# Performance work log

Hardware: AMD Instinct MI355X
Metric: run time of the kernel (lower is better)

Reference implementation:

```python
import jax, jax.numpy as jnp
import numpy as np

NUM_HEADS = 8
FREQ_RATIO = 0.5

def setup_inputs() -> dict:
    key = jax.random.key(0)
    ks = jax.random.split(key, 4)
    B, T, J, C = 16, 256, 17, 512
    x = jax.random.normal(ks[0], (B, T, J, C), jnp.float32)
    w_qkv = jax.random.normal(ks[1], (3 * C, C), jnp.float32) * 0.02
    w_proj = jax.random.normal(ks[2], (C, C), jnp.float32) * 0.02
    b_proj = jnp.zeros((C,), jnp.float32)
    freq_gate = jnp.ones((1,), jnp.float32)
    return {"x": x, "w_qkv": w_qkv, "w_proj": w_proj, "b_proj": b_proj, "freq_gate": freq_gate}

def reference(x, w_qkv, w_proj, b_proj, freq_gate):
    B, T, J, C = x.shape
    H = NUM_HEADS
    hd = C // H
    scale = hd ** (-0.5)
    # qkv projection (no bias): [B,T,J,3,H,hd] -> [3,B,H,T,J,hd]
    qkv = (x @ w_qkv.T).reshape(B, T, J, 3, H, hd)
    qkv = jnp.transpose(qkv, (3, 0, 4, 1, 2, 5))
    q, k, v = qkv[0], qkv[1], qkv[2]
    # temporal layout: [B,H,J,T,hd]
    qt = jnp.swapaxes(q, 2, 3)
    kt = jnp.swapaxes(k, 2, 3)
    vt = jnp.swapaxes(v, 2, 3)
    # ---- time-domain temporal attention ----
    attn = jax.nn.softmax(jnp.einsum('bhjtd,bhjsd->bhjts', qt, kt) * scale, axis=-1)
    x_time = jnp.einsum('bhjts,bhjsd->bhjtd', attn, vt)
    x_time = jnp.transpose(x_time, (0, 3, 2, 1, 4)).reshape(B, T, J, C)
    # ---- frequency-domain temporal attention ----
    qf = jnp.fft.rfft(qt, axis=3)
    kf = jnp.fft.rfft(kt, axis=3)
    vf = jnp.fft.rfft(vt, axis=3)
    f_full = T // 2 + 1
    keep = max(1, int(f_full * FREQ_RATIO))  # low-frequency crop
    qf, kf, vf = qf[:, :, :, :keep], kf[:, :, :, :keep], vf[:, :, :, :keep]
    af = jnp.einsum('bhjfd,bhjgd->bhjfg', qf, jnp.conj(kf)) * scale  # complex [B,H,J,keep,keep]
    af = jax.nn.softmax(af.real, axis=-1) + 1j * jax.nn.softmax(af.imag, axis=-1)
    xf = jnp.einsum('bhjfg,bhjgd->bhjfd', af, vf)
    xf = jnp.pad(xf, ((0, 0), (0, 0), (0, 0), (0, f_full - keep), (0, 0)))  # zero-pad high freqs
    x_freq = jnp.fft.irfft(xf, n=T, axis=3)
    x_freq = jnp.transpose(x_freq, (0, 3, 2, 1, 4)).reshape(B, T, J, C)
    # ---- gated combine + output projection ----
    gate = jax.nn.sigmoid(freq_gate)[0]
    out = gate * x_freq + (1.0 - gate) * x_time
    return out @ w_proj.T + b_proj
```

## Files before the change

kernel.cpp:

```cpp
#include <hip/hip_runtime.h>
#include <hip/hip_fp16.h>
#include <math.h>

#define NB 16
#define TT 256
#define JJ 17
#define CC 512
#define HH 8
#define HD 64
#define MROWS (NB*TT*JJ)
#define QTILE 16384
#define NTILES (NB*HH*JJ)
#define NQKV 35651584

#define FP 68
#define FHALF 4352
#define W0 0.0245436926061702596f

typedef __attribute__((ext_vector_type(8))) short i16x8;
typedef __attribute__((ext_vector_type(8))) _Float16 f16x8;
typedef __attribute__((ext_vector_type(4))) float f32x4;

__device__ __forceinline__ unsigned short f2h(float f) {
    return (unsigned short)__half_as_ushort(__float2half(f));
}
__device__ __forceinline__ float h2f(unsigned short u) {
    return __half2float(__ushort_as_half(u));
}

#define GLD16(gp, lp) __builtin_amdgcn_global_load_lds( \
    (__attribute__((address_space(1))) void*)(gp), \
    (__attribute__((address_space(3))) void*)(lp), 16, 0, 0)

__global__ __launch_bounds__(256) void conv16_k(
    const float* __restrict__ s, unsigned short* __restrict__ d, int n8)
{
    for (int i = blockIdx.x*256 + threadIdx.x; i < n8; i += gridDim.x*256) {
        float4 a = ((const float4*)s)[i*2];
        float4 b = ((const float4*)s)[i*2+1];
        i16x8 h;
        h[0] = (short)f2h(a.x); h[1] = (short)f2h(a.y);
        h[2] = (short)f2h(a.z); h[3] = (short)f2h(a.w);
        h[4] = (short)f2h(b.x); h[5] = (short)f2h(b.y);
        h[6] = (short)f2h(b.z); h[7] = (short)f2h(b.w);
        ((i16x8*)d)[i] = h;
    }
}

__global__ __launch_bounds__(256) void prep_k(
    const float* __restrict__ wq, const float* __restrict__ wp,
    unsigned short* __restrict__ wqh, unsigned short* __restrict__ wph,
    unsigned short* __restrict__ Whi, unsigned short* __restrict__ Wlo,
    unsigned short* __restrict__ WIhi)
{
    const int b = blockIdx.x;
    const int tid = threadIdx.x;
    if (b < 512) {
        const float* s = (b < 384) ? wq : wp;
        unsigned short* d = (b < 384) ? wqh : wph;
        int i = (b < 384 ? b : b - 384)*256 + tid;
        float4 a = ((const float4*)s)[i*2];
        float4 bb = ((const float4*)s)[i*2+1];
        i16x8 h;
        h[0] = (short)f2h(a.x); h[1] = (short)f2h(a.y);
        h[2] = (short)f2h(a.z); h[3] = (short)f2h(a.w);
        h[4] = (short)f2h(bb.x); h[5] = (short)f2h(bb.y);
        h[6] = (short)f2h(bb.z); h[7] = (short)f2h(bb.w);
        ((i16x8*)d)[i] = h;
    } else if (b < 640) {
        const int r = b - 512;
        const int t = tid;
        int idx = ((r & 63) * t) & 255;
        float sv, cv;
        sincosf(W0 * (float)idx, &sv, &cv);
        float val = (r < 64) ? cv : -sv;
        unsigned short h = f2h(val);
        Whi[r*256 + t] = h;
        Wlo[r*256 + t] = f2h(val - h2f(h));
    } else {
        int idx = (b - 640)*256 + tid;
        int t = idx >> 7;
        int f = idx & 127;
        int fr = f & 63;
        int ii = (t * fr) & 255;
        float sv, cv;
        sincosf(W0 * (float)ii, &sv, &cv);
        float cf = (fr == 0 && f < 64) ? 0.5f : 1.f;
        float val = ((f < 64) ? cv : -sv) * cf * (2.f / 256.f);
        WIhi[t*128 + f] = f2h(val);
    }
}

__global__ __launch_bounds__(256) void gemm_qkv_k(
    const unsigned short* __restrict__ A, const unsigned short* __restrict__ B,
    unsigned short* __restrict__ qp, unsigned short* __restrict__ kp,
    unsigned short* __restrict__ vp)
{
    __shared__ unsigned short Sh[128*128];
    unsigned short* Ah = Sh;
    unsigned short* Bh = Sh + 128*64;
    const int tid = threadIdx.x;
    const int lane = tid & 63;
    const int lo = lane & 15, hi = lane >> 4;
    const int wv = tid >> 6;
    const int wr = wv >> 1, wc = wv & 1;
    const int bid = blockIdx.x;
    const int wrk = (bid & 7) * 816 + (bid >> 3);
    const int col0 = (wrk % 12) * 128;
    const int row0 = (wrk / 12) * 128;

    f32x4 acc[4][4];
    #pragma unroll
    for (int rb = 0; rb < 4; ++rb)
        #pragma unroll
        for (int cb = 0; cb < 4; ++cb) acc[rb][cb] = (f32x4){0.f,0.f,0.f,0.f};

    for (int k0 = 0; k0 < 512; k0 += 64) {
        #pragma unroll
        for (int c = 0; c < 4; ++c) {
            int e = c*2048 + tid*8;
            int r = e >> 6, cc = e & 63;
            int ccs = cc ^ ((r & 7) << 3);
            size_t offA = (size_t)(row0 + r)*512 + k0 + ccs;
            size_t offB = (size_t)(col0 + r)*512 + k0 + ccs;
            GLD16(A + offA, (char*)Ah + c*4096 + tid*16);
            GLD16(B + offB, (char*)Bh + c*4096 + tid*16);
        }
        __syncthreads();
        #pragma unroll
        for (int ks = 0; ks < 2; ++ks) {
            f16x8 af[4], bf[4];
            #pragma unroll
            for (int rb = 0; rb < 4; ++rb) {
                int row = wr*64 + rb*16 + lo;
                int col = (ks*32 + hi*8) ^ ((row & 7) << 3);
                af[rb] = *(const f16x8*)&Ah[row*64 + col];
            }
            #pragma unroll
            for (int cb = 0; cb < 4; ++cb) {
                int row = wc*64 + cb*16 + lo;
                int col = (ks*32 + hi*8) ^ ((row & 7) << 3);
                bf[cb] = *(const f16x8*)&Bh[row*64 + col];
            }
            #pragma unroll
            for (int rb = 0; rb < 4; ++rb)
                #pragma unroll
                for (int cb = 0; cb < 4; ++cb)
                    acc[rb][cb] = __builtin_amdgcn_mfma_f32_16x16x32_f16(
                        af[rb], bf[cb], acc[rb][cb], 0, 0, 0);
        }
        __syncthreads();
    }

    #pragma unroll
    for (int cb = 0; cb < 4; ++cb) {
        int n0 = col0 + wc*64 + cb*16;
        float scl = ((n0 >> 9) == 0) ? 0.125f : 1.f;
        #pragma unroll
        for (int rb = 0; rb < 4; ++rb)
            #pragma unroll
            for (int r = 0; r < 4; ++r) {
                int row = wr*64 + rb*16 + hi*4 + r;
                int col = wc*64 + cb*16 + lo;
                Sh[row*128 + (col ^ ((row & 7) << 3))] = f2h(acc[rb][cb][r]*scl);
            }
    }
    __syncthreads();

    {
        const int grp = lane >> 3;
        const int d0 = (lane & 7) * 8;
        #pragma unroll
        for (int it = 0; it < 8; ++it) {
            int p = it*32 + wv*8 + grp;
            int row = p >> 1;
            int half = p & 1;
            int m = row0 + row;
            int bb = m / (TT*JJ);
            int rem = m - bb*(TT*JJ);
            int t = rem / JJ;
            int j = rem - t*JJ;
            int n0 = col0 + half*64;
            int g = n0 >> 9;
            unsigned short* dst0 = (g == 0) ? qp : (g == 1) ? kp : vp;
            int h = (n0 >> 6) & 7;
            unsigned short* dst = dst0 +
                ((((size_t)bb*HH + h)*JJ + j)*TT + t)*HD + d0;
            i16x8 vls = *(const i16x8*)&Sh[row*128 + ((half*64 + d0) ^ ((row & 7) << 3))];
            *(i16x8*)dst = vls;
        }
    }
}

__global__ __launch_bounds__(256) void gemm_proj_k(
    const unsigned short* __restrict__ A, const unsigned short* __restrict__ B,
    const float* __restrict__ bias, float* __restrict__ out)
{
    __shared__ unsigned short Ah[128*64];
    __shared__ unsigned short Bh[128*64];
    const int tid = threadIdx.x;
    const int lane = tid & 63;
    const int lo = lane & 15, hi = lane >> 4;
    const int wv = tid >> 6;
    const int wr = wv >> 1, wc = wv & 1;
    const int bid = blockIdx.x;
    const int wrk = (bid & 7) * 272 + (bid >> 3);
    const int col0 = (wrk % 4) * 128;
    const int row0 = (wrk / 4) * 128;

    f32x4 acc[4][4];
    #pragma unroll
    for (int rb = 0; rb < 4; ++rb)
        #pragma unroll
        for (int cb = 0; cb < 4; ++cb) acc[rb][cb] = (f32x4){0.f,0.f,0.f,0.f};

    for (int k0 = 0; k0 < 512; k0 += 64) {
        #pragma unroll
        for (int c = 0; c < 4; ++c) {
            int e = c*2048 + tid*8;
            int r = e >> 6, cc = e & 63;
            int ccs = cc ^ ((r & 7) << 3);
            size_t offA = (size_t)(row0 + r)*512 + k0 + ccs;
            size_t offB = (size_t)(col0 + r)*512 + k0 + ccs;
            GLD16(A + offA, (char*)Ah + c*4096 + tid*16);
            GLD16(B + offB, (char*)Bh + c*4096 + tid*16);
        }
        __syncthreads();
        #pragma unroll
        for (int ks = 0; ks < 2; ++ks) {
            f16x8 af[4], bf[4];
            #pragma unroll
            for (int rb = 0; rb < 4; ++rb) {
                int row = wr*64 + rb*16 + lo;
                int col = (ks*32 + hi*8) ^ ((row & 7) << 3);
                af[rb] = *(const f16x8*)&Ah[row*64 + col];
            }
            #pragma unroll
            for (int cb = 0; cb < 4; ++cb) {
                int row = wc*64 + cb*16 + lo;
                int col = (ks*32 + hi*8) ^ ((row & 7) << 3);
                bf[cb] = *(const f16x8*)&Bh[row*64 + col];
            }
            #pragma unroll
            for (int rb = 0; rb < 4; ++rb)
                #pragma unroll
                for (int cb = 0; cb < 4; ++cb)
                    acc[rb][cb] = __builtin_amdgcn_mfma_f32_16x16x32_f16(
                        af[rb], bf[cb], acc[rb][cb], 0, 0, 0);
        }
        __syncthreads();
    }

    #pragma unroll
    for (int cb = 0; cb < 4; ++cb) {
        int n = col0 + wc*64 + cb*16 + lo;
        float bv = bias[n];
        #pragma unroll
        for (int rb = 0; rb < 4; ++rb)
            #pragma unroll
            for (int r = 0; r < 4; ++r) {
                int m = row0 + wr*64 + rb*16 + hi*4 + r;
                out[(size_t)m*512 + n] = acc[rb][cb][r] + bv;
            }
    }
}

#define VTP 264
#define PPW 40

__global__ __launch_bounds__(256, 2) void attn_time_k(
    const unsigned short* __restrict__ q, const unsigned short* __restrict__ k,
    const unsigned short* __restrict__ v, const float* __restrict__ fg,
    unsigned short* __restrict__ y)
{
    __shared__ unsigned short VT[64 * VTP];
    __shared__ unsigned short PL[4 * 64 * PPW];

    const int bid = blockIdx.x;
    const int b = bid / (HH*JJ);
    const int h = (bid / JJ) % HH;
    const int j = bid % JJ;
    const size_t base = (size_t)bid * QTILE;

    const int tid = threadIdx.x;
    const int w = tid >> 6;
    const int lane = tid & 63;
    const int lo = lane & 15;
    const int hi = lane >> 4;

    {
        const unsigned short* vptr = v + base + (size_t)tid * HD;
        #pragma unroll
        for (int d0 = 0; d0 < 64; d0 += 8) {
            i16x8 vv = *(const i16x8*)(vptr + d0);
            #pragma unroll
            for (int e = 0; e < 8; ++e)
                VT[(d0+e)*VTP + tid] = (unsigned short)vv[e];
        }
    }
    __syncthreads();

    f16x8 qf[4][2];
    #pragma unroll
    for (int rb = 0; rb < 4; ++rb)
        #pragma unroll
        for (int dc = 0; dc < 2; ++dc)
            qf[rb][dc] = *(const f16x8*)(q + base + (size_t)(w*64 + rb*16 + lo)*HD + dc*32 + hi*8);

    f32x4 o[4][4];
    #pragma unroll
    for (int rb = 0; rb < 4; ++rb)
        #pragma unroll
        for (int cd = 0; cd < 4; ++cd) o[rb][cd] = (f32x4){0.f,0.f,0.f,0.f};
    float rs[4][4];
    #pragma unroll
    for (int rb = 0; rb < 4; ++rb)
        #pragma unroll
        for (int r = 0; r < 4; ++r) rs[rb][r] = 0.f;

    unsigned short* Pw = PL + w * 64 * PPW;

    for (int st = 0; st < 8; ++st) {
        const int s0 = st * 32;
        f16x8 kf[2][2];
        #pragma unroll
        for (int cb = 0; cb < 2; ++cb)
            #pragma unroll
            for (int dc = 0; dc < 2; ++dc)
                kf[cb][dc] = *(const f16x8*)(k + base + (size_t)(s0 + cb*16 + lo)*HD + dc*32 + hi*8);

        #pragma unroll
        for (int rb = 0; rb < 4; ++rb) {
            #pragma unroll
            for (int cb = 0; cb < 2; ++cb) {
                f32x4 acc = (f32x4){0.f,0.f,0.f,0.f};
                acc = __builtin_amdgcn_mfma_f32_16x16x32_f16(qf[rb][0], kf[cb][0], acc, 0, 0, 0);
                acc = __builtin_amdgcn_mfma_f32_16x16x32_f16(qf[rb][1], kf[cb][1], acc, 0, 0, 0);
                #pragma unroll
                for (int r = 0; r < 4; ++r) {
                    float p = __expf(acc[r]);
                    rs[rb][r] += p;
                    Pw[(rb*16 + hi*4 + r)*PPW + cb*16 + lo] = f2h(p);
                }
            }
        }

        f16x8 pa[4];
        #pragma unroll
        for (int rb = 0; rb < 4; ++rb)
            pa[rb] = *(const f16x8*)&Pw[(rb*16 + lo)*PPW + hi*8];
        f16x8 bv[4];
        #pragma unroll
        for (int cd = 0; cd < 4; ++cd)
            bv[cd] = *(const f16x8*)&VT[(cd*16 + lo)*VTP + s0 + hi*8];
        #pragma unroll
        for (int rb = 0; rb < 4; ++rb)
            #pragma unroll
            for (int cd = 0; cd < 4; ++cd)
                o[rb][cd] = __builtin_amdgcn_mfma_f32_16x16x32_f16(pa[rb], bv[cd], o[rb][cd], 0, 0, 0);
    }

    #pragma unroll
    for (int off = 1; off < 16; off <<= 1)
        #pragma unroll
        for (int rb = 0; rb < 4; ++rb)
            #pragma unroll
            for (int r = 0; r < 4; ++r)
                rs[rb][r] += __shfl_xor(rs[rb][r], off, 64);

    const float gate = 1.f / (1.f + __expf(-fg[0]));
    const float wt = 1.f - gate;
    #pragma unroll
    for (int rb = 0; rb < 4; ++rb) {
        #pragma unroll
        for (int r = 0; r < 4; ++r) {
            const int t = w*64 + rb*16 + hi*4 + r;
            const float sc = wt / rs[rb][r];
            unsigned short* yp = y + (((size_t)b*TT + t)*JJ + j)*CC + h*HD;
            #pragma unroll
            for (int cd = 0; cd < 4; ++cd)
                yp[cd*16 + lo] = f2h(o[rb][cd][r] * sc);
        }
    }
}

#define XP 280

__global__ __launch_bounds__(256) void dft_k(
    unsigned short* __restrict__ planes, const unsigned short* __restrict__ Whi,
    const unsigned short* __restrict__ Wlo)
{
    __shared__ unsigned short Xh[64*XP];
    unsigned short* src = planes + (size_t)blockIdx.y*NQKV + (size_t)blockIdx.x*QTILE;
    const int tid = threadIdx.x;
    const int w = tid >> 6;
    const int lane = tid & 63;
    const int qd = (tid >> 4) & 3;
    const int rr = tid & 15;
    const int lo = lane & 15, hi = lane >> 4;

    #pragma unroll
    for (int p = 0; p < 16; ++p) {
        const int t = p*16 + 4*w + qd;
        ushort4 x4 = *(const ushort4*)&src[t*64 + 4*rr];
        unsigned int a0 = x4.x, a1 = x4.y, a2 = x4.z, a3 = x4.w;
        unsigned int t01 = (unsigned)__shfl_xor((int)((qd&1) ? a0 : a1), 16, 64);
        unsigned int t23 = (unsigned)__shfl_xor((int)((qd&1) ? a2 : a3), 16, 64);
        if (qd&1) { a0 = t01; a2 = t23; } else { a1 = t01; a3 = t23; }
        unsigned int u01 = (unsigned)__shfl_xor((int)((qd&2) ? a0 : a2), 32, 64);
        unsigned int u23 = (unsigned)__shfl_xor((int)((qd&2) ? a1 : a3), 32, 64);
        if (qd&2) { a0 = u01; a1 = u23; } else { a2 = u01; a3 = u23; }
        const int dd = 4*rr + qd;
        const int tb = p*16 + 4*w;
        ushort4 hv;
        hv.x = (unsigned short)a0; hv.y = (unsigned short)a1;
        hv.z = (unsigned short)a2; hv.w = (unsigned short)a3;
        *(ushort4*)&Xh[dd*XP + tb] = hv;
    }
    __syncthreads();

    f32x4 acc[2][4];
    #pragma unroll
    for (int rb = 0; rb < 2; ++rb)
        #pragma unroll
        for (int cd = 0; cd < 4; ++cd) acc[rb][cd] = (f32x4){0.f,0.f,0.f,0.f};

    for (int ks = 0; ks < 8; ++ks) {
        const int k0 = ks*32;
        f16x8 ah[2], al[2];
        #pragma unroll
        for (int rb = 0; rb < 2; ++rb) {
            int r = w*32 + rb*16 + lo;
            ah[rb] = *(const f16x8*)&Whi[r*256 + k0 + hi*8];
            al[rb] = *(const f16x8*)&Wlo[r*256 + k0 + hi*8];
        }
        f16x8 bh[4];
        #pragma unroll
        for (int cd = 0; cd < 4; ++cd) {
            int d = cd*16 + lo;
            bh[cd] = *(const f16x8*)&Xh[d*XP + k0 + hi*8];
        }
        #pragma unroll
        for (int rb = 0; rb < 2; ++rb)
            #pragma unroll
            for (int cd = 0; cd < 4; ++cd) {
                acc[rb][cd] = __builtin_amdgcn_mfma_f32_16x16x32_f16(
                    ah[rb], bh[cd], acc[rb][cd], 0, 0, 0);
                acc[rb][cd] = __builtin_amdgcn_mfma_f32_16x16x32_f16(
                    al[rb], bh[cd], acc[rb][cd], 0, 0, 0);
            }
    }

    #pragma unroll
    for (int rb = 0; rb < 2; ++rb) {
        #pragma unroll
        for (int r = 0; r < 4; ++r) {
            int row = w*32 + rb*16 + hi*4 + r;
            unsigned short* dst = (row < 64) ? (src + row*64)
                                             : (src + 4096 + (row-64)*64);
            #pragma unroll
            for (int cd = 0; cd < 4; ++cd)
                dst[cd*16 + lo] = f2h(acc[rb][cd][r]);
        }
    }
}

#define XFP 136

__global__ __launch_bounds__(256) void freqtail_k(
    unsigned short* __restrict__ qfp, const unsigned short* __restrict__ kfp,
    const unsigned short* __restrict__ vfp, const unsigned short* __restrict__ WIhi,
    const float* __restrict__ fg, unsigned short* __restrict__ y)
{
    extern __shared__ float lds[];
    float* A = lds;
    float* B = lds + 2*FHALF;

    const int tid = threadIdx.x;
    const int tile = blockIdx.x;
    const int b = tile / (HH*JJ);
    const int h = (tile / JJ) % HH;
    const int j = tile % JJ;
    const unsigned short* qf = qfp + (size_t)tile * QTILE;
    const unsigned short* kf = kfp + (size_t)tile * QTILE;
    const unsigned short* vf = vfp + (size_t)tile * QTILE;

    #pragma unroll
    for (int p = 0; p < 4; ++p) {
        int idx = p*256 + tid;
        int e8 = idx*8;
        int part = e8 >> 12;
        int row = (e8 >> 6) & 63;
        int col = e8 & 63;
        i16x8 qv = *(const i16x8*)(qf + e8);
        i16x8 kv = *(const i16x8*)(kf + e8);
        float* ap = A + part*FHALF + row*FP + col;
        float* bp = B + part*FHALF + row*FP + col;
        #pragma unroll
        for (int e = 0; e < 8; ++e) {
            ap[e] = h2f((unsigned short)qv[e]);
            bp[e] = h2f((unsigned short)kv[e]);
        }
    }
    __syncthreads();

    const int fy = tid >> 4;
    const int gl = tid & 15;

    float cR[4][4], cI[4][4];
    #pragma unroll
    for (int i = 0; i < 4; ++i)
        #pragma unroll
        for (int gi = 0; gi < 4; ++gi) { cR[i][gi] = 0.f; cI[i][gi] = 0.f; }

    for (int d4 = 0; d4 < 16; ++d4) {
        float4 qr[4], qi[4], kr[4], ki[4];
        #pragma unroll
        for (int i = 0; i < 4; ++i) {
            int f = fy + 16*i;
            qr[i] = *(const float4*)(A + f*FP + d4*4);
            qi[i] = *(const float4*)(A + FHALF + f*FP + d4*4);
            int g = gl + 16*i;
            kr[i] = *(const float4*)(B + g*FP + d4*4);
            ki[i] = *(const float4*)(B + FHALF + g*FP + d4*4);
        }
        #pragma unroll
        for (int i = 0; i < 4; ++i)
            #pragma unroll
            for (int gi = 0; gi < 4; ++gi) {
                float r = cR[i][gi], m = cI[i][gi];
                r = fmaf(qr[i].x, kr[gi].x, r); r = fmaf(qi[i].x, ki[gi].x, r);
                r = fmaf(qr[i].y, kr[gi].y, r); r = fmaf(qi[i].y, ki[gi].y, r);
                r = fmaf(qr[i].z, kr[gi].z, r); r = fmaf(qi[i].z, ki[gi].z, r);
                r = fmaf(qr[i].w, kr[gi].w, r); r = fmaf(qi[i].w, ki[gi].w, r);
                m = fmaf(qi[i].x, kr[gi].x, m); m = fmaf(-qr[i].x, ki[gi].x, m);
                m = fmaf(qi[i].y, kr[gi].y, m); m = fmaf(-qr[i].y, ki[gi].y, m);
                m = fmaf(qi[i].z, kr[gi].z, m); m = fmaf(-qr[i].z, ki[gi].z, m);
                m = fmaf(qi[i].w, kr[gi].w, m); m = fmaf(-qr[i].w, ki[gi].w, m);
                cR[i][gi] = r; cI[i][gi] = m;
            }
    }
    __syncthreads();

    #pragma unroll
    for (int i = 0; i < 4; ++i)
        #pragma unroll
        for (int gi = 0; gi < 4; ++gi) {
            A[(fy + 16*i)*FP + gl + 16*gi]         = cR[i][gi];
            A[FHALF + (fy + 16*i)*FP + gl + 16*gi] = cI[i][gi];
        }
    #pragma unroll
    for (int p = 0; p < 4; ++p) {
        int idx = p*256 + tid;
        int e8 = idx*8;
        int part = e8 >> 12;
        int row = (e8 >> 6) & 63;
        int col = e8 & 63;
        i16x8 vv = *(const i16x8*)(vf + e8);
        float* bp = B + part*FHALF + row*FP + col;
        #pragma unroll
        for (int e = 0; e < 8; ++e) bp[e] = h2f((unsigned short)vv[e]);
    }
    __syncthreads();

    if (tid < 128) {
        float* row = A + (tid >> 6)*FHALF + (tid & 63)*FP;
        float mx = row[0];
        for (int g2 = 1; g2 < 64; ++g2) mx = fmaxf(mx, row[g2]);
        float sum = 0.f;
        for (int g2 = 0; g2 < 64; ++g2) { float e = __expf(row[g2]-mx); row[g2] = e; sum += e; }
        float inv = 1.f / sum;
        for (int g2 = 0; g2 < 64; ++g2) row[g2] *= inv;
    }
    __syncthreads();

    float xR[4][4], xI[4][4];
    #pragma unroll
    for (int i = 0; i < 4; ++i)
        #pragma unroll
        for (int cmp = 0; cmp < 4; ++cmp) { xR[i][cmp] = 0.f; xI[i][cmp] = 0.f; }

    for (int g2 = 0; g2 < 64; ++g2) {
        float4 vr = *(const float4*)(B + g2*FP + gl*4);
        float4 vi = *(const float4*)(B + FHALF + g2*FP + gl*4);
        #pragma unroll
        for (int i = 0; i < 4; ++i) {
            float sr = A[(fy + 16*i)*FP + g2];
            float si = A[FHALF + (fy + 16*i)*FP + g2];
            xR[i][0] = fmaf(sr, vr.x, fmaf(-si, vi.x, xR[i][0]));
            xI[i][0] = fmaf(sr, vi.x, fmaf( si, vr.x, xI[i][0]));
            xR[i][1] = fmaf(sr, vr.y, fmaf(-si, vi.y, xR[i][1]));
            xI[i][1] = fmaf(sr, vi.y, fmaf( si, vr.y, xI[i][1]));
            xR[i][2] = fmaf(sr, vr.z, fmaf(-si, vi.z, xR[i][2]));
            xI[i][2] = fmaf(sr, vi.z, fmaf( si, vr.z, xI[i][2]));
            xR[i][3] = fmaf(sr, vr.w, fmaf(-si, vi.w, xR[i][3]));
            xI[i][3] = fmaf(sr, vi.w, fmaf( si, vr.w, xI[i][3]));
        }
    }
    __syncthreads();

    unsigned short* XT = (unsigned short*)B;
    #pragma unroll
    for (int i = 0; i < 4; ++i) {
        int f = fy + 16*i;
        #pragma unroll
        for (int e = 0; e < 4; ++e) {
            XT[(gl*4+e)*XFP + f]      = f2h(xR[i][e]);
            XT[(gl*4+e)*XFP + 64 + f] = f2h(xI[i][e]);
        }
    }
    __syncthreads();

    const int w = tid >> 6;
    const int lane = tid & 63;
    const int lo = lane & 15, hi = lane >> 4;

    f32x4 acc[4][4];
    #pragma unroll
    for (int rb = 0; rb < 4; ++rb)
        #pragma unroll
        for (int cd = 0; cd < 4; ++cd) acc[rb][cd] = (f32x4){0.f,0.f,0.f,0.f};

    #pragma unroll
    for (int ks = 0; ks < 4; ++ks) {
        const int k0 = ks*32;
        f16x8 ah[4];
        #pragma unroll
        for (int rb = 0; rb < 4; ++rb) {
            int row = w*64 + rb*16 + lo;
            ah[rb] = *(const f16x8*)&WIhi[row*128 + k0 + hi*8];
        }
        f16x8 bt[4];
        #pragma unroll
        for (int cd = 0; cd < 4; ++cd) {
            int d = cd*16 + lo;
            bt[cd] = *(const f16x8*)&XT[d*XFP + k0 + hi*8];
        }
        #pragma unroll
        for (int rb = 0; rb < 4; ++rb)
            #pragma unroll
            for (int cd = 0; cd < 4; ++cd)
                acc[rb][cd] = __builtin_amdgcn_mfma_f32_16x16x32_f16(
                    ah[rb], bt[cd], acc[rb][cd], 0, 0, 0);
    }

    const float gate = 1.f / (1.f + __expf(-fg[0]));
    #pragma unroll
    for (int rb = 0; rb < 4; ++rb) {
        #pragma unroll
        for (int r = 0; r < 4; ++r) {
            int t = w*64 + rb*16 + hi*4 + r;
            unsigned short* yp = y + (((size_t)b*TT + t)*JJ + j)*CC + h*HD;
            #pragma unroll
            for (int cd = 0; cd < 4; ++cd) {
                int d = cd*16 + lo;
                yp[d] = f2h(fmaf(gate, acc[rb][cd][r], h2f(yp[d])));
            }
        }
    }
}

extern "C" void kernel_launch(void* const* d_in, const int* in_sizes, int n_in,
                              void* d_out, int out_size, void* d_ws, size_t ws_size,
                              hipStream_t stream) {
    const float* x      = (const float*)d_in[0];
    const float* w_qkv  = (const float*)d_in[1];
    const float* w_proj = (const float*)d_in[2];
    const float* b_proj = (const float*)d_in[3];
    const float* fg     = (const float*)d_in[4];
    float* out = (float*)d_out;

    unsigned short* qp = (unsigned short*)d_ws;
    unsigned short* kp = qp + NQKV;
    unsigned short* vp = kp + NQKV;
    unsigned short* xh = vp + NQKV;
    unsigned short* y  = xh + NQKV;
    unsigned short* wph = y + NQKV;
    unsigned short* wqh = (unsigned short*)d_out;
    unsigned short* Whi  = wqh + 1536*512;
    unsigned short* Wlo  = Whi + 128*256;
    unsigned short* WIhi = Wlo + 128*256;

    (void)hipFuncSetAttribute((const void*)freqtail_k,
                              hipFuncAttributeMaxDynamicSharedMemorySize, 4*FHALF*4);

    conv16_k<<<2048, 256, 0, stream>>>(x, xh, NQKV/8);
    prep_k<<<768, 256, 0, stream>>>(w_qkv, w_proj, wqh, wph, Whi, Wlo, WIhi);

    gemm_qkv_k<<<6528, 256, 0, stream>>>(xh, wqh, qp, kp, vp);
    attn_time_k<<<NTILES, 256, 0, stream>>>(qp, kp, vp, fg, y);
    dft_k<<<dim3(NTILES, 3), 256, 0, stream>>>(qp, Whi, Wlo);
    freqtail_k<<<NTILES, 256, 4*FHALF*4, stream>>>(qp, kp, vp, WIhi, fg, y);

    gemm_proj_k<<<2176, 256, 0, stream>>>(y, wph, b_proj, out);
}
```

Before: 688.0 us.

## Move frequency-domain attention to fp16 MFMA and swizzle time-attention V layout

```diff
diff --git a/kernel.cpp b/kernel.cpp
--- a/kernel.cpp
+++ b/kernel.cpp
@@ -13,8 +13,6 @@
 #define NTILES (NB*HH*JJ)
 #define NQKV 35651584
 
-#define FP 68
-#define FHALF 4352
 #define W0 0.0245436926061702596f
 
 typedef __attribute__((ext_vector_type(8))) short i16x8;
@@ -265,15 +263,14 @@
     }
 }
 
-#define VTP 264
 #define PPW 40
 
-__global__ __launch_bounds__(256, 2) void attn_time_k(
+__global__ __launch_bounds__(256, 3) void attn_time_k(
     const unsigned short* __restrict__ q, const unsigned short* __restrict__ k,
     const unsigned short* __restrict__ v, const float* __restrict__ fg,
     unsigned short* __restrict__ y)
 {
-    __shared__ unsigned short VT[64 * VTP];
+    __shared__ unsigned short VT[64 * 256];
     __shared__ unsigned short PL[4 * 64 * PPW];
 
     const int bid = blockIdx.x;
@@ -294,8 +291,10 @@
         for (int d0 = 0; d0 < 64; d0 += 8) {
             i16x8 vv = *(const i16x8*)(vptr + d0);
             #pragma unroll
-            for (int e = 0; e < 8; ++e)
-                VT[(d0+e)*VTP + tid] = (unsigned short)vv[e];
+            for (int e = 0; e < 8; ++e) {
+                int row = d0 + e;
+                VT[row*256 + (tid ^ ((row & 7) << 3))] = (unsigned short)vv[e];
+            }
         }
     }
     __syncthreads();
@@ -351,8 +350,10 @@
             pa[rb] = *(const f16x8*)&Pw[(rb*16 + lo)*PPW + hi*8];
         f16x8 bv[4];
         #pragma unroll
-        for (int cd = 0; cd < 4; ++cd)
-            bv[cd] = *(const f16x8*)&VT[(cd*16 + lo)*VTP + s0 + hi*8];
+        for (int cd = 0; cd < 4; ++cd) {
+            int row = cd*16 + lo;
+            bv[cd] = *(const f16x8*)&VT[row*256 + ((s0 + hi*8) ^ ((row & 7) << 3))];
+        }
         #pragma unroll
         for (int rb = 0; rb < 4; ++rb)
             #pragma unroll
@@ -465,16 +466,16 @@
     }
 }
 
+#define FQP 72
 #define XFP 136
 
 __global__ __launch_bounds__(256) void freqtail_k(
-    unsigned short* __restrict__ qfp, const unsigned short* __restrict__ kfp,
+    const unsigned short* __restrict__ qfp, const unsigned short* __restrict__ kfp,
     const unsigned short* __restrict__ vfp, const unsigned short* __restrict__ WIhi,
     const float* __restrict__ fg, unsigned short* __restrict__ y)
 {
-    extern __shared__ float lds[];
-    float* A = lds;
-    float* B = lds + 2*FHALF;
+    __shared__ unsigned short S1[128*FQP];
+    __shared__ unsigned short S2[128*FQP];
 
     const int tid = threadIdx.x;
     const int tile = blockIdx.x;
@@ -485,135 +486,158 @@
     const unsigned short* kf = kfp + (size_t)tile * QTILE;
     const unsigned short* vf = vfp + (size_t)tile * QTILE;
 
-    #pragma unroll
-    for (int p = 0; p < 4; ++p) {
-        int idx = p*256 + tid;
-        int e8 = idx*8;
-        int part = e8 >> 12;
-        int row = (e8 >> 6) & 63;
-        int col = e8 & 63;
-        i16x8 qv = *(const i16x8*)(qf + e8);
-        i16x8 kv = *(const i16x8*)(kf + e8);
-        float* ap = A + part*FHALF + row*FP + col;
-        float* bp = B + part*FHALF + row*FP + col;
-        #pragma unroll
-        for (int e = 0; e < 8; ++e) {
-            ap[e] = h2f((unsigned short)qv[e]);
-            bp[e] = h2f((unsigned short)kv[e]);
-        }
-    }
-    __syncthreads();
-
-    const int fy = tid >> 4;
-    const int gl = tid & 15;
-
-    float cR[4][4], cI[4][4];
-    #pragma unroll
-    for (int i = 0; i < 4; ++i)
-        #pragma unroll
-        for (int gi = 0; gi < 4; ++gi) { cR[i][gi] = 0.f; cI[i][gi] = 0.f; }
-
-    for (int d4 = 0; d4 < 16; ++d4) {
-        float4 qr[4], qi[4], kr[4], ki[4];
-        #pragma unroll
-        for (int i = 0; i < 4; ++i) {
-            int f = fy + 16*i;
-            qr[i] = *(const float4*)(A + f*FP + d4*4);
-            qi[i] = *(const float4*)(A + FHALF + f*FP + d4*4);
-            int g = gl + 16*i;
-            kr[i] = *(const float4*)(B + g*FP + d4*4);
-            ki[i] = *(const float4*)(B + FHALF + g*FP + d4*4);
-        }
-        #pragma unroll
-        for (int i = 0; i < 4; ++i)
-            #pragma unroll
-            for (int gi = 0; gi < 4; ++gi) {
-                float r = cR[i][gi], m = cI[i][gi];
-                r = fmaf(qr[i].x, kr[gi].x, r); r = fmaf(qi[i].x, ki[gi].x, r);
-                r = fmaf(qr[i].y, kr[gi].y, r); r = fmaf(qi[i].y, ki[gi].y, r);
-                r = fmaf(qr[i].z, kr[gi].z, r); r = fmaf(qi[i].z, ki[gi].z, r);
-                r = fmaf(qr[i].w, kr[gi].w, r); r = fmaf(qi[i].w, ki[gi].w, r);
-                m = fmaf(qi[i].x, kr[gi].x, m); m = fmaf(-qr[i].x, ki[gi].x, m);
-                m = fmaf(qi[i].y, kr[gi].y, m); m = fmaf(-qr[i].y, ki[gi].y, m);
-                m = fmaf(qi[i].z, kr[gi].z, m); m = fmaf(-qr[i].z, ki[gi].z, m);
-                m = fmaf(qi[i].w, kr[gi].w, m); m = fmaf(-qr[i].w, ki[gi].w, m);
-                cR[i][gi] = r; cI[i][gi] = m;
-            }
-    }
-    __syncthreads();
-
-    #pragma unroll
-    for (int i = 0; i < 4; ++i)
-        #pragma unroll
-        for (int gi = 0; gi < 4; ++gi) {
-            A[(fy + 16*i)*FP + gl + 16*gi]         = cR[i][gi];
-            A[FHALF + (fy + 16*i)*FP + gl + 16*gi] = cI[i][gi];
-        }
-    #pragma unroll
-    for (int p = 0; p < 4; ++p) {
-        int idx = p*256 + tid;
-        int e8 = idx*8;
-        int part = e8 >> 12;
-        int row = (e8 >> 6) & 63;
-        int col = e8 & 63;
-        i16x8 vv = *(const i16x8*)(vf + e8);
-        float* bp = B + part*FHALF + row*FP + col;
-        #pragma unroll
-        for (int e = 0; e < 8; ++e) bp[e] = h2f((unsigned short)vv[e]);
-    }
-    __syncthreads();
-
-    if (tid < 128) {
-        float* row = A + (tid >> 6)*FHALF + (tid & 63)*FP;
-        float mx = row[0];
-        for (int g2 = 1; g2 < 64; ++g2) mx = fmaxf(mx, row[g2]);
-        float sum = 0.f;
-        for (int g2 = 0; g2 < 64; ++g2) { float e = __expf(row[g2]-mx); row[g2] = e; sum += e; }
-        float inv = 1.f / sum;
-        for (int g2 = 0; g2 < 64; ++g2) row[g2] *= inv;
-    }
-    __syncthreads();
-
-    float xR[4][4], xI[4][4];
-    #pragma unroll
-    for (int i = 0; i < 4; ++i)
-        #pragma unroll
-        for (int cmp = 0; cmp < 4; ++cmp) { xR[i][cmp] = 0.f; xI[i][cmp] = 0.f; }
-
-    for (int g2 = 0; g2 < 64; ++g2) {
-        float4 vr = *(const float4*)(B + g2*FP + gl*4);
-        float4 vi = *(const float4*)(B + FHALF + g2*FP + gl*4);
-        #pragma unroll
-        for (int i = 0; i < 4; ++i) {
-            float sr = A[(fy + 16*i)*FP + g2];
-            float si = A[FHALF + (fy + 16*i)*FP + g2];
-            xR[i][0] = fmaf(sr, vr.x, fmaf(-si, vi.x, xR[i][0]));
-            xI[i][0] = fmaf(sr, vi.x, fmaf( si, vr.x, xI[i][0]));
-            xR[i][1] = fmaf(sr, vr.y, fmaf(-si, vi.y, xR[i][1]));
-            xI[i][1] = fmaf(sr, vi.y, fmaf( si, vr.y, xI[i][1]));
-            xR[i][2] = fmaf(sr, vr.z, fmaf(-si, vi.z, xR[i][2]));
-            xI[i][2] = fmaf(sr, vi.z, fmaf( si, vr.z, xI[i][2]));
-            xR[i][3] = fmaf(sr, vr.w, fmaf(-si, vi.w, xR[i][3]));
-            xI[i][3] = fmaf(sr, vi.w, fmaf( si, vr.w, xI[i][3]));
-        }
-    }
-    __syncthreads();
-
-    unsigned short* XT = (unsigned short*)B;
-    #pragma unroll
-    for (int i = 0; i < 4; ++i) {
-        int f = fy + 16*i;
-        #pragma unroll
-        for (int e = 0; e < 4; ++e) {
-            XT[(gl*4+e)*XFP + f]      = f2h(xR[i][e]);
-            XT[(gl*4+e)*XFP + 64 + f] = f2h(xI[i][e]);
-        }
-    }
-    __syncthreads();
-
     const int w = tid >> 6;
     const int lane = tid & 63;
     const int lo = lane & 15, hi = lane >> 4;
+    const int comp = w >> 1;
+    const int fr0 = (w & 1) * 32;
+
+    #pragma unroll
+    for (int p = 0; p < 4; ++p) {
+        int e8 = (p*256 + tid) * 8;
+        int row = e8 >> 6, col = e8 & 63;
+        *(i16x8*)&S1[row*FQP + col] = *(const i16x8*)(qf + e8);
+        *(i16x8*)&S2[row*FQP + col] = *(const i16x8*)(kf + e8);
+    }
+    __syncthreads();
+
+    f32x4 accA[2][4], accB[2][4];
+    #pragma unroll
+    for (int rb = 0; rb < 2; ++rb)
+        #pragma unroll
+        for (int cb = 0; cb < 4; ++cb) {
+            accA[rb][cb] = (f32x4){0.f,0.f,0.f,0.f};
+            accB[rb][cb] = (f32x4){0.f,0.f,0.f,0.f};
+        }
+    #pragma unroll
+    for (int ks = 0; ks < 2; ++ks) {
+        f16x8 qA[2], qB[2];
+        #pragma unroll
+        for (int rb = 0; rb < 2; ++rb) {
+            int fr = fr0 + rb*16 + lo;
+            qA[rb] = *(const f16x8*)&S1[(comp*64 + fr)*FQP + ks*32 + hi*8];
+            qB[rb] = *(const f16x8*)&S1[((1-comp)*64 + fr)*FQP + ks*32 + hi*8];
+        }
+        f16x8 kr[4], ki[4];
+        #pragma unroll
+        for (int cb = 0; cb < 4; ++cb) {
+            int g = cb*16 + lo;
+            kr[cb] = *(const f16x8*)&S2[g*FQP + ks*32 + hi*8];
+            ki[cb] = *(const f16x8*)&S2[(64 + g)*FQP + ks*32 + hi*8];
+        }
+        #pragma unroll
+        for (int rb = 0; rb < 2; ++rb)
+            #pragma unroll
+            for (int cb = 0; cb < 4; ++cb) {
+                accA[rb][cb] = __builtin_amdgcn_mfma_f32_16x16x32_f16(
+                    qA[rb], kr[cb], accA[rb][cb], 0, 0, 0);
+                accB[rb][cb] = __builtin_amdgcn_mfma_f32_16x16x32_f16(
+                    qB[rb], ki[cb], accB[rb][cb], 0, 0, 0);
+            }
+    }
+    __syncthreads();
+
+    const float sgn = comp ? -1.f : 1.f;
+    float pv[2][4][4];
+    float inv[2][4];
+    #pragma unroll
+    for (int rb = 0; rb < 2; ++rb) {
+        #pragma unroll
+        for (int r = 0; r < 4; ++r) {
+            float m = -3.0e38f;
+            #pragma unroll
+            for (int cb = 0; cb < 4; ++cb) {
+                float vv = accA[rb][cb][r] + sgn*accB[rb][cb][r];
+                pv[rb][cb][r] = vv;
+                m = fmaxf(m, vv);
+            }
+            #pragma unroll
+            for (int off = 1; off < 16; off <<= 1)
+                m = fmaxf(m, __shfl_xor(m, off, 64));
+            float s = 0.f;
+            #pragma unroll
+            for (int cb = 0; cb < 4; ++cb) {
+                float e = __expf(pv[rb][cb][r] - m);
+                pv[rb][cb][r] = e;
+                s += e;
+            }
+            #pragma unroll
+            for (int off = 1; off < 16; off <<= 1)
+                s += __shfl_xor(s, off, 64);
+            inv[rb][r] = 1.f / s;
+        }
+    }
+    #pragma unroll
+    for (int rb = 0; rb < 2; ++rb)
+        #pragma unroll
+        for (int r = 0; r < 4; ++r)
+            #pragma unroll
+            for (int cb = 0; cb < 4; ++cb)
+                S1[(w*32 + rb*16 + hi*4 + r)*FQP + cb*16 + lo] =
+                    f2h(pv[rb][cb][r] * inv[rb][r]);
+
+    #pragma unroll
+    for (int p = 0; p < 4; ++p) {
+        int e8 = (p*256 + tid) * 8;
+        int srow = e8 >> 6;
+        int c2 = srow >> 6, g = srow & 63, d0 = e8 & 63;
+        i16x8 vv = *(const i16x8*)(vf + e8);
+        #pragma unroll
+        for (int e = 0; e < 8; ++e)
+            S2[(c2*64 + d0 + e)*FQP + g] = (unsigned short)vv[e];
+    }
+    __syncthreads();
+
+    f32x4 xA[2][4], xB[2][4];
+    #pragma unroll
+    for (int rb = 0; rb < 2; ++rb)
+        #pragma unroll
+        for (int cd = 0; cd < 4; ++cd) {
+            xA[rb][cd] = (f32x4){0.f,0.f,0.f,0.f};
+            xB[rb][cd] = (f32x4){0.f,0.f,0.f,0.f};
+        }
+    #pragma unroll
+    for (int ks = 0; ks < 2; ++ks) {
+        f16x8 pA[2], pB[2];
+        #pragma unroll
+        for (int rb = 0; rb < 2; ++rb) {
+            int fr = fr0 + rb*16 + lo;
+            pA[rb] = *(const f16x8*)&S1[fr*FQP + ks*32 + hi*8];
+            pB[rb] = *(const f16x8*)&S1[(64 + fr)*FQP + ks*32 + hi*8];
+        }
+        f16x8 bA[4], bB[4];
+        #pragma unroll
+        for (int cd = 0; cd < 4; ++cd) {
+            int d = cd*16 + lo;
+            bA[cd] = *(const f16x8*)&S2[(comp*64 + d)*FQP + ks*32 + hi*8];
+            bB[cd] = *(const f16x8*)&S2[((1-comp)*64 + d)*FQP + ks*32 + hi*8];
+        }
+        #pragma unroll
+        for (int rb = 0; rb < 2; ++rb)
+            #pragma unroll
+            for (int cd = 0; cd < 4; ++cd) {
+                xA[rb][cd] = __builtin_amdgcn_mfma_f32_16x16x32_f16(
+                    pA[rb], bA[cd], xA[rb][cd], 0, 0, 0);
+                xB[rb][cd] = __builtin_amdgcn_mfma_f32_16x16x32_f16(
+                    pB[rb], bB[cd], xB[rb][cd], 0, 0, 0);
+            }
+    }
+    __syncthreads();
+
+    const float sgn2 = comp ? 1.f : -1.f;
+    unsigned short* XT = S1;
+    #pragma unroll
+    for (int rb = 0; rb < 2; ++rb)
+        #pragma unroll
+        for (int cd = 0; cd < 4; ++cd)
+            #pragma unroll
+            for (int r = 0; r < 4; ++r) {
+                int f = fr0 + rb*16 + hi*4 + r;
+                int d = cd*16 + lo;
+                XT[d*XFP + comp*64 + f] =
+                    f2h(xA[rb][cd][r] + sgn2*xB[rb][cd][r]);
+            }
+    __syncthreads();
 
     f32x4 acc[4][4];
     #pragma unroll
@@ -681,16 +705,13 @@
     unsigned short* Wlo  = Whi + 128*256;
     unsigned short* WIhi = Wlo + 128*256;
 
-    (void)hipFuncSetAttribute((const void*)freqtail_k,
-                              hipFuncAttributeMaxDynamicSharedMemorySize, 4*FHALF*4);
-
     conv16_k<<<2048, 256, 0, stream>>>(x, xh, NQKV/8);
     prep_k<<<768, 256, 0, stream>>>(w_qkv, w_proj, wqh, wph, Whi, Wlo, WIhi);
 
     gemm_qkv_k<<<6528, 256, 0, stream>>>(xh, wqh, qp, kp, vp);
     attn_time_k<<<NTILES, 256, 0, stream>>>(qp, kp, vp, fg, y);
     dft_k<<<dim3(NTILES, 3), 256, 0, stream>>>(qp, Whi, Wlo);
-    freqtail_k<<<NTILES, 256, 4*FHALF*4, stream>>>(qp, kp, vp, WIhi, fg, y);
+    freqtail_k<<<NTILES, 256, 0, stream>>>(qp, kp, vp, WIhi, fg, y);
 
     gemm_proj_k<<<2176, 256, 0, stream>>>(y, wph, b_proj, out);
 }
```

Result: faster. 586.1 us (-14.8%).
